# Optimization experiments

Measured on AMD Instinct MI355X. Metric: run time of the kernel, lower is better.

## Reference

```python
import jax, jax.numpy as jnp
import numpy as np
from jax import lax

DN = ('NHWC', 'HWIO', 'NHWC')  # conv dimension numbers


def setup_inputs() -> dict:
    key = jax.random.key(0)
    ks = jax.random.split(key, 10)
    B, H, W, C, F, E = 16, 32, 32, 128, 128, 8
    G = F * (H // 2) * (W // 2)  # 32768, gating flatten size
    return {
        'x': jax.random.normal(ks[0], (B, H, W, C), jnp.float32),
        'eps_kernel': jax.random.normal(ks[1], (3, 3, C, F, E), jnp.float32),
        'eps_gate': jax.random.normal(ks[2], (B, E), jnp.float32),
        'expert_mu': jax.random.normal(ks[3], (3, 3, C, F, E), jnp.float32) * 0.05,
        'expert_rho': jax.random.normal(ks[4], (3, C, F, E), jnp.float32) * 0.01 - 6.0,
        'expert_bias': jax.random.normal(ks[5], (F, E), jnp.float32) * 0.01,
        'gating_kernel': jax.random.normal(ks[6], (3, 3, C, F), jnp.float32) * 0.05,
        'gating_bias': jax.random.normal(ks[7], (F,), jnp.float32) * 0.01,
        'gating_out_kernel': jax.random.normal(ks[8], (G, E), jnp.float32) * 0.01,
        'gating_out_bias': jax.random.normal(ks[9], (E,), jnp.float32) * 0.01,
    }


def reference(x, eps_kernel, eps_gate, expert_mu, expert_rho, expert_bias,
              gating_kernel, gating_bias, gating_out_kernel, gating_out_bias):
    GATING_NOISE_SIGMA = 1e-4
    TOP_K = 2
    B = x.shape[0]
    kh, kw, C, F, E = expert_mu.shape

    # Bayesian reparameterized expert kernels: rho shared over first kernel dim
    sigma = jax.nn.softplus(expert_rho)[None]               # [1,kw,C,F,E]
    kernel = expert_mu + sigma * eps_kernel                 # [kh,kw,C,F,E]

    # All-expert conv as one grouped conv via output-channel packing
    kern_flat = kernel.reshape(kh, kw, C, F * E)
    expert_out = lax.conv_general_dilated(x, kern_flat, (1, 1), 'SAME',
                                          dimension_numbers=DN)
    expert_out = expert_out.reshape(B, x.shape[1], x.shape[2], F, E)
    expert_out = expert_out + expert_bias                   # [B,H,W,F,E]

    # Gating path: conv -> 2x2 maxpool -> flatten -> dense -> noisy logits
    g = lax.conv_general_dilated(x, gating_kernel, (1, 1), 'SAME',
                                 dimension_numbers=DN) + gating_bias
    g = lax.reduce_window(g, -jnp.inf, lax.max,
                          (1, 2, 2, 1), (1, 2, 2, 1), 'VALID')
    logits = g.reshape(B, -1) @ gating_out_kernel + gating_out_bias  # [B,E]
    logits = logits + GATING_NOISE_SIGMA * eps_gate

    # noisy top-k gating: softmax over selected experts, zero elsewhere
    top_vals, top_idx = lax.top_k(logits, TOP_K)
    top_w = jax.nn.softmax(top_vals, axis=-1)
    gates = jnp.zeros((B, E), logits.dtype).at[
        jnp.arange(B)[:, None], top_idx].set(top_w)

    # combine experts weighted by gates, broadcast over spatial dims
    out = jnp.einsum('bhwfe,be->bhwf', expert_out, gates)
    return out
```

## Files before the change

kernel.cpp:

```cpp
#include <hip/hip_runtime.h>
#include <cmath>

#define B_ 16
#define H_ 32
#define W_ 32
#define C_ 128
#define F_ 128
#define KSZ (9*C_*F_)
#define NKS 36
#define FRAG_ELE 4096

typedef __bf16 bf16;
typedef __bf16 bf16x4 __attribute__((ext_vector_type(4)));
typedef __bf16 bf16x8 __attribute__((ext_vector_type(8)));
typedef float  f32x4  __attribute__((ext_vector_type(4)));

__device__ __forceinline__ float softplus_f(float v) {
  return log1pf(expf(-fabsf(v))) + fmaxf(v, 0.f);
}

__device__ __forceinline__ void top2_gates_f(const float* lg, float* gl) {
  int i0 = 0;
  #pragma unroll
  for (int e = 1; e < 8; ++e) if (lg[e] > lg[i0]) i0 = e;
  int i1 = (i0 == 0) ? 1 : 0;
  #pragma unroll
  for (int e = 0; e < 8; ++e) if (e != i0 && lg[e] > lg[i1]) i1 = e;
  float m  = fmaxf(lg[i0], lg[i1]);
  float e0 = expf(lg[i0] - m), e1 = expf(lg[i1] - m);
  float s  = e0 + e1;
  #pragma unroll
  for (int e = 0; e < 8; ++e) gl[e] = 0.f;
  gl[i0] = e0 / s; gl[i1] = e1 / s;
}

__device__ __forceinline__ float logit_f(const float* part, const float* gob,
                                         const float* epsg, int bb, int e) {
  float s = 0.f;
  #pragma unroll
  for (int hb = 0; hb < 16; ++hb) s += part[(bb*16 + hb)*8 + e];
  return s + gob[e] + 1e-4f * epsg[bb*8 + e];
}

__device__ __forceinline__ void block_map_f(int bid, int* b, int* hb) {
  *b  = (bid & 7) * 2 + (bid >> 7);
  *hb = (bid >> 3) & 15;
}

template<int NVAR>
__global__ __launch_bounds__(512, 2) void conv_k(
    const float* __restrict__ x,
    const bf16* __restrict__ Bhi, const bf16* __restrict__ Blo,
    const float* __restrict__ gb,
    const float* __restrict__ Wg,
    const float* __restrict__ part,
    const float* __restrict__ gob,
    const float* __restrict__ epsg,
    const float* __restrict__ ebias,
    float* __restrict__ outv)
{
  int b, hb;
  block_map_f(blockIdx.x, &b, &hb);
  const int t = threadIdx.x;

  __shared__ bf16 xs[NVAR*4*34*128];
  __shared__ float red[8][8];
  __shared__ float gl8[8];

  for (int v = t; v < 4*34*32; v += 512) {
    int c4   = v & 31;
    int col  = (v >> 5) % 34;
    int rowi = (v >> 5) / 34;
    int row  = hb*2 - 1 + rowi;
    int w    = col - 1;
    float4 xv = make_float4(0.f, 0.f, 0.f, 0.f);
    if (row >= 0 && row < H_ && w >= 0 && w < W_)
      xv = *(const float4*)&x[((b*H_ + row)*W_ + w)*C_ + c4*4];
    float vv[4] = {xv.x, xv.y, xv.z, xv.w};
    bf16x4 h4, l4;
    #pragma unroll
    for (int j = 0; j < 4; ++j) {
      h4[j] = (bf16)vv[j];
      if (NVAR == 2) l4[j] = (bf16)(vv[j] - (float)h4[j]);
    }
    int base = ((rowi*34 + col)*256 + c4*8) ^ ((col & 7) << 4);
    *(bf16x4*)((char*)xs + base) = h4;
    if (NVAR == 2) *(bf16x4*)((char*)xs + 34816 + base) = l4;
  }
  if (NVAR == 1 && t == 0) {
    float lg[8], gg[8];
    #pragma unroll
    for (int e = 0; e < 8; ++e) lg[e] = logit_f(part, gob, epsg, b, e);
    top2_gates_f(lg, gg);
    #pragma unroll
    for (int e = 0; e < 8; ++e) gl8[e] = gg[e];
  }
  __syncthreads();

  const int l    = t & 63;
  const int wid  = t >> 6;
  const int mpar = wid & 1;
  const int nf0  = (wid >> 1) << 1;
  const int r15  = l & 15;
  const int q    = l >> 4;

  f32x4 acc00 = {0.f,0.f,0.f,0.f}, acc01 = acc00, acc10 = acc00, acc11 = acc00;

  const bf16* Bh = Bhi + (NVAR == 1 ? (size_t)b * KSZ : (size_t)0);
  const size_t bgo = (size_t)(nf0*512 + l*8);

  bf16x8 s0h0,s0h1,s0l0,s0l1, s1h0,s1h1,s1l0,s1l1, s2h0,s2h1,s2l0,s2l1;

#define LOADB(S, KS_) do {                                                  \
    int kk_ = (KS_); if (kk_ > NKS-1) kk_ = NKS-1;                          \
    size_t o_ = bgo + (size_t)kk_ * FRAG_ELE;                               \
    S##h0 = *(const bf16x8*)(Bh + o_);                                      \
    S##h1 = *(const bf16x8*)(Bh + o_ + 512);                                \
    if (NVAR == 2) {                                                        \
      S##l0 = *(const bf16x8*)(Blo + o_);                                   \
      S##l1 = *(const bf16x8*)(Blo + o_ + 512);                             \
    }                                                                       \
  } while (0)

#define MFMA16(a, bb_, c) __builtin_amdgcn_mfma_f32_16x16x32_bf16(a, bb_, c, 0, 0, 0)

#define COMPUTE(S, KS_) do {                                                \
    const int khkw_ = (KS_) >> 2;                                           \
    const int kh_ = khkw_ / 3, kw_ = khkw_ % 3;                             \
    const int c0_ = ((KS_) & 3) << 5;                                       \
    const int col_ = mpar*16 + r15 + kw_;                                   \
    const int off_ = ((kh_*34 + col_)*256 + (c0_ + q*8)*2) ^ ((col_ & 7) << 4); \
    bf16x8 a0_ = *(const bf16x8*)((const char*)xs + off_);                  \
    bf16x8 a1_ = *(const bf16x8*)((const char*)xs + off_ + 8704);           \
    __builtin_amdgcn_s_setprio(1);                                          \
    acc00 = MFMA16(a0_, S##h0, acc00);                                      \
    acc01 = MFMA16(a0_, S##h1, acc01);                                      \
    acc10 = MFMA16(a1_, S##h0, acc10);                                      \
    acc11 = MFMA16(a1_, S##h1, acc11);                                      \
    if (NVAR == 2) {                                                        \
      bf16x8 g0_ = *(const bf16x8*)((const char*)xs + 34816 + off_);        \
      bf16x8 g1_ = *(const bf16x8*)((const char*)xs + 34816 + off_ + 8704); \
      acc00 = MFMA16(g0_, S##h0, acc00);                                    \
      acc01 = MFMA16(g0_, S##h1, acc01);                                    \
      acc10 = MFMA16(g1_, S##h0, acc10);                                    \
      acc11 = MFMA16(g1_, S##h1, acc11);                                    \
      acc00 = MFMA16(a0_, S##l0, acc00);                                    \
      acc01 = MFMA16(a0_, S##l1, acc01);                                    \
      acc10 = MFMA16(a1_, S##l0, acc10);                                    \
      acc11 = MFMA16(a1_, S##l1, acc11);                                    \
    }                                                                       \
    __builtin_amdgcn_s_setprio(0);                                          \
  } while (0)

  LOADB(s0, 0); LOADB(s1, 1); LOADB(s2, 2);
  for (int ks = 0; ks < NKS; ks += 3) {
    COMPUTE(s0, ks);   LOADB(s0, ks+3);
    COMPUTE(s1, ks+1); LOADB(s1, ks+4);
    COMPUTE(s2, ks+2); LOADB(s2, ks+5);
  }
#undef LOADB
#undef COMPUTE

  if (NVAR == 1) {
    const int f0 = nf0*16 + r15;
    float bv0 = 0.f, bv1 = 0.f;
    #pragma unroll
    for (int e = 0; e < 8; ++e) {
      bv0 += gl8[e] * ebias[f0*8 + e];
      bv1 += gl8[e] * ebias[(f0+16)*8 + e];
    }
    #pragma unroll
    for (int mi = 0; mi < 2; ++mi) {
      const int h = hb*2 + mi;
      #pragma unroll
      for (int r = 0; r < 4; ++r) {
        const int wo = mpar*16 + q*4 + r;
        float* o = &outv[((b*H_ + h)*W_ + wo)*F_];
        o[f0]      = (mi ? acc10[r] : acc00[r]) + bv0;
        o[f0 + 16] = (mi ? acc11[r] : acc01[r]) + bv1;
      }
    }
  } else {
    float pr[8] = {0,0,0,0,0,0,0,0};
    #pragma unroll
    for (int ni = 0; ni < 2; ++ni) {
      const int f = (nf0 + ni)*16 + r15;
      const float bv = gb[f];
      #pragma unroll
      for (int pp = 0; pp < 2; ++pp) {
        float m0 = ni ? fmaxf(acc01[2*pp], acc01[2*pp+1])
                      : fmaxf(acc00[2*pp], acc00[2*pp+1]);
        float m1 = ni ? fmaxf(acc11[2*pp], acc11[2*pp+1])
                      : fmaxf(acc10[2*pp], acc10[2*pp+1]);
        float pm = fmaxf(m0, m1) + bv;
        const int pw = mpar*8 + q*2 + pp;
        const float* wr = &Wg[(size_t)((hb*16 + pw)*128 + f) * 8];
        float4 wA = *(const float4*)wr;
        float4 wB = *(const float4*)(wr + 4);
        pr[0] += pm*wA.x; pr[1] += pm*wA.y; pr[2] += pm*wA.z; pr[3] += pm*wA.w;
        pr[4] += pm*wB.x; pr[5] += pm*wB.y; pr[6] += pm*wB.z; pr[7] += pm*wB.w;
      }
    }
    #pragma unroll
    for (int o = 32; o > 0; o >>= 1)
      #pragma unroll
      for (int e = 0; e < 8; ++e) pr[e] += __shfl_down(pr[e], o);
    if (l == 0)
      #pragma unroll
      for (int e = 0; e < 8; ++e) red[wid][e] = pr[e];
    __syncthreads();
    if (t < 8) {
      float s = 0.f;
      #pragma unroll
      for (int w = 0; w < 8; ++w) s += red[w][t];
      outv[(b*16 + hb)*8 + t] = s;
    }
  }
}

__global__ __launch_bounds__(256) void effk_k(
    const float* __restrict__ mu, const float* __restrict__ rho,
    const float* __restrict__ eps,
    const float* __restrict__ part, const float* __restrict__ gob,
    const float* __restrict__ epsg,
    bf16* __restrict__ Bg)
{
  const int ks  = blockIdx.x >> 3;
  const int rem = blockIdx.x & 7;
  const int t   = threadIdx.x;
  const int nf  = (rem & 1)*4 + (t >> 6);
  const int bq  = (rem >> 1) * 4;

  __shared__ float lgs[4][8];
  __shared__ float gl[4][8];
  if (t < 32) lgs[t >> 3][t & 7] = logit_f(part, gob, epsg, bq + (t >> 3), t & 7);
  __syncthreads();
  if (t < 4) top2_gates_f(lgs[t], gl[t]);
  __syncthreads();

  const int l    = t & 63;
  const int khkw = ks >> 2;
  const int kw   = khkw % 3;
  const int f    = nf*16 + (l & 15);
  const int cb   = (ks & 3)*32 + (l >> 4)*8;

  bf16x8 ob[4];
  #pragma unroll
  for (int j = 0; j < 8; ++j) {
    const int c = cb + j;
    const float* mp = &mu [(size_t)((khkw*C_ + c)*F_ + f) * 8];
    const float* ep = &eps[(size_t)((khkw*C_ + c)*F_ + f) * 8];
    const float* rp = &rho[(size_t)((kw  *C_ + c)*F_ + f) * 8];
    float kv[8];
    #pragma unroll
    for (int e = 0; e < 8; ++e)
      kv[e] = mp[e] + softplus_f(rp[e]) * ep[e];
    #pragma unroll
    for (int bb = 0; bb < 4; ++bb) {
      float s = 0.f;
      #pragma unroll
      for (int e = 0; e < 8; ++e) s += gl[bb][e] * kv[e];
      ob[bb][j] = (bf16)s;
    }
  }
  #pragma unroll
  for (int bb = 0; bb < 4; ++bb) {
    size_t o = (size_t)(bq + bb)*KSZ + (size_t)ks*FRAG_ELE + nf*512 + l*8;
    *(bf16x8*)&Bg[o] = ob[bb];
  }
}

__global__ __launch_bounds__(512) void gkconv_k(
    const float* __restrict__ gk, bf16* __restrict__ bgh, bf16* __restrict__ bgl)
{
  __shared__ float tile[32*129];
  const int ks   = blockIdx.x;
  const int khkw = ks >> 2;
  const int cb   = (ks & 3)*32;
  const int t    = threadIdx.x;

  for (int v = t; v < 1024; v += 512) {
    int c  = v >> 5;
    int f4 = (v & 31) * 4;
    float4 val = *(const float4*)&gk[(size_t)(khkw*C_ + cb + c)*F_ + f4];
    float* dst = &tile[c*129 + f4];
    dst[0] = val.x; dst[1] = val.y; dst[2] = val.z; dst[3] = val.w;
  }
  __syncthreads();

  const int nf = t >> 6, l = t & 63;
  const int f  = nf*16 + (l & 15);
  bf16x8 h8, l8;
  #pragma unroll
  for (int j = 0; j < 8; ++j) {
    int c = (l >> 4)*8 + j;
    float v = tile[c*129 + f];
    bf16 h = (bf16)v;
    h8[j] = h;
    l8[j] = (bf16)(v - (float)h);
  }
  *(bf16x8*)&bgh[(size_t)ks*FRAG_ELE + t*8] = h8;
  *(bf16x8*)&bgl[(size_t)ks*FRAG_ELE + t*8] = l8;
}

extern "C" void kernel_launch(void* const* d_in, const int* in_sizes, int n_in,
                              void* d_out, int out_size, void* d_ws, size_t ws_size,
                              hipStream_t stream) {
  const float* x    = (const float*)d_in[0];
  const float* epsk = (const float*)d_in[1];
  const float* epsg = (const float*)d_in[2];
  const float* mu   = (const float*)d_in[3];
  const float* rho  = (const float*)d_in[4];
  const float* ebias= (const float*)d_in[5];
  const float* gk   = (const float*)d_in[6];
  const float* gb   = (const float*)d_in[7];
  const float* gok  = (const float*)d_in[8];
  const float* gob  = (const float*)d_in[9];
  float* out = (float*)d_out;

  char* ws = (char*)d_ws;
  bf16*  bgh  = (bf16*) (ws);
  bf16*  bgl  = (bf16*) (ws + 294912);
  bf16*  bge  = (bf16*) (ws + 589824);
  float* part = (float*)(ws + 5308416);

  gkconv_k<<<NKS, 512, 0, stream>>>(gk, bgh, bgl);
  conv_k<2><<<B_*16, 512, 0, stream>>>(x, bgh, bgl, gb, gok,
                                       nullptr, nullptr, nullptr, nullptr, part);
  effk_k<<<NKS*8, 256, 0, stream>>>(mu, rho, epsk, part, gob, epsg, bge);
  conv_k<1><<<B_*16, 512, 0, stream>>>(x, bge, bge, nullptr, nullptr,
                                       part, gob, epsg, ebias, out);
}
```

Measured before the change: 65.72 us.

## Split conv blocks over output-channel halves and redistribute waves across rows

Doubles the conv grid so each block computes only half of the output channels, and gives each wave one output row with 32 channels instead of two rows. This halves the per-wave accumulators and raises the launch-bounds occupancy hint, so all CUs get more concurrent waves. The gating max-pool now combines the two rows through shared memory, and the partial-logit buffer grows to 32 slices per batch. The cost is that each block stages the input tile into LDS twice as often overall, and the pooling path adds extra barriers.

```diff
diff --git a/kernel.cpp b/kernel.cpp
--- a/kernel.cpp
+++ b/kernel.cpp
@@ -38,17 +38,18 @@
                                          const float* epsg, int bb, int e) {
   float s = 0.f;
   #pragma unroll
-  for (int hb = 0; hb < 16; ++hb) s += part[(bb*16 + hb)*8 + e];
+  for (int p = 0; p < 32; ++p) s += part[(bb*32 + p)*8 + e];
   return s + gob[e] + 1e-4f * epsg[bb*8 + e];
 }
 
-__device__ __forceinline__ void block_map_f(int bid, int* b, int* hb) {
-  *b  = (bid & 7) * 2 + (bid >> 7);
+__device__ __forceinline__ void block_map_f(int bid, int* b, int* hb, int* nh) {
+  *b  = (bid & 7) * 2 + (bid >> 8);
   *hb = (bid >> 3) & 15;
+  *nh = (bid >> 7) & 1;
 }
 
 template<int NVAR>
-__global__ __launch_bounds__(512, 2) void conv_k(
+__global__ __launch_bounds__(512, 4) void conv_k(
     const float* __restrict__ x,
     const bf16* __restrict__ Bhi, const bf16* __restrict__ Blo,
     const float* __restrict__ gb,
@@ -59,8 +60,8 @@
     const float* __restrict__ ebias,
     float* __restrict__ outv)
 {
-  int b, hb;
-  block_map_f(blockIdx.x, &b, &hb);
+  int b, hb, nh;
+  block_map_f(blockIdx.x, &b, &hb, &nh);
   const int t = threadIdx.x;
 
   __shared__ bf16 xs[NVAR*4*34*128];
@@ -99,15 +100,17 @@
 
   const int l    = t & 63;
   const int wid  = t >> 6;
-  const int mpar = wid & 1;
-  const int nf0  = (wid >> 1) << 1;
+  const int mq   = wid & 3;
+  const int hl   = mq >> 1;
+  const int wh   = mq & 1;
+  const int nfp  = wid >> 2;
   const int r15  = l & 15;
   const int q    = l >> 4;
 
-  f32x4 acc00 = {0.f,0.f,0.f,0.f}, acc01 = acc00, acc10 = acc00, acc11 = acc00;
+  f32x4 acc0 = {0.f,0.f,0.f,0.f}, acc1 = acc0;
 
   const bf16* Bh = Bhi + (NVAR == 1 ? (size_t)b * KSZ : (size_t)0);
-  const size_t bgo = (size_t)(nf0*512 + l*8);
+  const size_t bgo = (size_t)((nh*4 + nfp*2)*512 + l*8);
 
   bf16x8 s0h0,s0h1,s0l0,s0l1, s1h0,s1h1,s1l0,s1l1, s2h0,s2h1,s2l0,s2l1;
 
@@ -128,26 +131,19 @@
     const int khkw_ = (KS_) >> 2;                                           \
     const int kh_ = khkw_ / 3, kw_ = khkw_ % 3;                             \
     const int c0_ = ((KS_) & 3) << 5;                                       \
-    const int col_ = mpar*16 + r15 + kw_;                                   \
-    const int off_ = ((kh_*34 + col_)*256 + (c0_ + q*8)*2) ^ ((col_ & 7) << 4); \
-    bf16x8 a0_ = *(const bf16x8*)((const char*)xs + off_);                  \
-    bf16x8 a1_ = *(const bf16x8*)((const char*)xs + off_ + 8704);           \
+    const int col_ = wh*16 + r15 + kw_;                                     \
+    const int off_ = (((kh_ + hl)*34 + col_)*256 + (c0_ + q*8)*2)           \
+                     ^ ((col_ & 7) << 4);                                   \
+    bf16x8 a_hi = *(const bf16x8*)((const char*)xs + off_);                 \
     __builtin_amdgcn_s_setprio(1);                                          \
-    acc00 = MFMA16(a0_, S##h0, acc00);                                      \
-    acc01 = MFMA16(a0_, S##h1, acc01);                                      \
-    acc10 = MFMA16(a1_, S##h0, acc10);                                      \
-    acc11 = MFMA16(a1_, S##h1, acc11);                                      \
+    acc0 = MFMA16(a_hi, S##h0, acc0);                                       \
+    acc1 = MFMA16(a_hi, S##h1, acc1);                                       \
     if (NVAR == 2) {                                                        \
-      bf16x8 g0_ = *(const bf16x8*)((const char*)xs + 34816 + off_);        \
-      bf16x8 g1_ = *(const bf16x8*)((const char*)xs + 34816 + off_ + 8704); \
-      acc00 = MFMA16(g0_, S##h0, acc00);                                    \
-      acc01 = MFMA16(g0_, S##h1, acc01);                                    \
-      acc10 = MFMA16(g1_, S##h0, acc10);                                    \
-      acc11 = MFMA16(g1_, S##h1, acc11);                                    \
-      acc00 = MFMA16(a0_, S##l0, acc00);                                    \
-      acc01 = MFMA16(a0_, S##l1, acc01);                                    \
-      acc10 = MFMA16(a1_, S##l0, acc10);                                    \
-      acc11 = MFMA16(a1_, S##l1, acc11);                                    \
+      bf16x8 a_lo = *(const bf16x8*)((const char*)xs + 34816 + off_);       \
+      acc0 = MFMA16(a_lo, S##h0, acc0);                                     \
+      acc1 = MFMA16(a_lo, S##h1, acc1);                                     \
+      acc0 = MFMA16(a_hi, S##l0, acc0);                                     \
+      acc1 = MFMA16(a_hi, S##l1, acc1);                                     \
     }                                                                       \
     __builtin_amdgcn_s_setprio(0);                                          \
   } while (0)
@@ -162,43 +158,52 @@
 #undef COMPUTE
 
   if (NVAR == 1) {
-    const int f0 = nf0*16 + r15;
+    const int f0 = nh*64 + nfp*32 + r15;
     float bv0 = 0.f, bv1 = 0.f;
     #pragma unroll
     for (int e = 0; e < 8; ++e) {
       bv0 += gl8[e] * ebias[f0*8 + e];
       bv1 += gl8[e] * ebias[(f0+16)*8 + e];
     }
-    #pragma unroll
-    for (int mi = 0; mi < 2; ++mi) {
-      const int h = hb*2 + mi;
-      #pragma unroll
-      for (int r = 0; r < 4; ++r) {
-        const int wo = mpar*16 + q*4 + r;
-        float* o = &outv[((b*H_ + h)*W_ + wo)*F_];
-        o[f0]      = (mi ? acc10[r] : acc00[r]) + bv0;
-        o[f0 + 16] = (mi ? acc11[r] : acc01[r]) + bv1;
+    const int h = hb*2 + hl;
+    #pragma unroll
+    for (int r = 0; r < 4; ++r) {
+      const int wo = wh*16 + q*4 + r;
+      float* o = &outv[((b*H_ + h)*W_ + wo)*F_];
+      o[f0]      = acc0[r] + bv0;
+      o[f0 + 16] = acc1[r] + bv1;
+    }
+  } else {
+    __syncthreads();
+    float* hpool = (float*)xs;
+    #pragma unroll
+    for (int ni = 0; ni < 2; ++ni) {
+      const int fl = nfp*32 + ni*16 + r15;
+      #pragma unroll
+      for (int pp = 0; pp < 2; ++pp) {
+        float mw = ni ? fmaxf(acc1[2*pp], acc1[2*pp+1])
+                      : fmaxf(acc0[2*pp], acc0[2*pp+1]);
+        const int pw = wh*8 + q*2 + pp;
+        hpool[(hl*16 + pw)*64 + fl] = mw;
       }
     }
-  } else {
+    __syncthreads();
     float pr[8] = {0,0,0,0,0,0,0,0};
-    #pragma unroll
-    for (int ni = 0; ni < 2; ++ni) {
-      const int f = (nf0 + ni)*16 + r15;
-      const float bv = gb[f];
-      #pragma unroll
-      for (int pp = 0; pp < 2; ++pp) {
-        float m0 = ni ? fmaxf(acc01[2*pp], acc01[2*pp+1])
-                      : fmaxf(acc00[2*pp], acc00[2*pp+1]);
-        float m1 = ni ? fmaxf(acc11[2*pp], acc11[2*pp+1])
-                      : fmaxf(acc10[2*pp], acc10[2*pp+1]);
-        float pm = fmaxf(m0, m1) + bv;
-        const int pw = mpar*8 + q*2 + pp;
-        const float* wr = &Wg[(size_t)((hb*16 + pw)*128 + f) * 8];
-        float4 wA = *(const float4*)wr;
-        float4 wB = *(const float4*)(wr + 4);
-        pr[0] += pm*wA.x; pr[1] += pm*wA.y; pr[2] += pm*wA.z; pr[3] += pm*wA.w;
-        pr[4] += pm*wB.x; pr[5] += pm*wB.y; pr[6] += pm*wB.z; pr[7] += pm*wB.w;
+    if (hl == 0) {
+      #pragma unroll
+      for (int ni = 0; ni < 2; ++ni) {
+        const int fl = nfp*32 + ni*16 + r15;
+        const float bv = gb[nh*64 + fl];
+        #pragma unroll
+        for (int pp = 0; pp < 2; ++pp) {
+          const int pw = wh*8 + q*2 + pp;
+          float pm = fmaxf(hpool[pw*64 + fl], hpool[(16 + pw)*64 + fl]) + bv;
+          const float* wr = &Wg[(size_t)((hb*16 + pw)*128 + nh*64 + fl) * 8];
+          float4 wA = *(const float4*)wr;
+          float4 wB = *(const float4*)(wr + 4);
+          pr[0] += pm*wA.x; pr[1] += pm*wA.y; pr[2] += pm*wA.z; pr[3] += pm*wA.w;
+          pr[4] += pm*wB.x; pr[5] += pm*wB.y; pr[6] += pm*wB.z; pr[7] += pm*wB.w;
+        }
       }
     }
     #pragma unroll
@@ -213,7 +218,7 @@
       float s = 0.f;
       #pragma unroll
       for (int w = 0; w < 8; ++w) s += red[w][t];
-      outv[(b*16 + hb)*8 + t] = s;
+      outv[(b*32 + hb*2 + nh)*8 + t] = s;
     }
   }
 }
@@ -325,9 +330,9 @@
   float* part = (float*)(ws + 5308416);
 
   gkconv_k<<<NKS, 512, 0, stream>>>(gk, bgh, bgl);
-  conv_k<2><<<B_*16, 512, 0, stream>>>(x, bgh, bgl, gb, gok,
-                                       nullptr, nullptr, nullptr, nullptr, part);
+  conv_k<2><<<512, 512, 0, stream>>>(x, bgh, bgl, gb, gok,
+                                     nullptr, nullptr, nullptr, nullptr, part);
   effk_k<<<NKS*8, 256, 0, stream>>>(mu, rho, epsk, part, gob, epsg, bge);
-  conv_k<1><<<B_*16, 512, 0, stream>>>(x, bge, bge, nullptr, nullptr,
-                                       part, gob, epsg, ebias, out);
-}
+  conv_k<1><<<512, 512, 0, stream>>>(x, bge, bge, nullptr, nullptr,
+                                     part, gob, epsg, ebias, out);
+}
```

Measured after the change: 78.62 us. 19.6% more time.

## Stage conv weight fragments through LDS with async global_load_lds pipeline

Applied to the files above, without the earlier changes.

The conv kernel now has each wave issue global_load_lds copies of one weight fragment per K-step into a ring buffer in shared memory. The pipeline is 6 deep for the expert conv and 3 deep for the gating conv, with vmcnt waits plus a block barrier each step. Previously each wave loaded its own fragments into registers, so every fragment was fetched twice, by both waves sharing an nf pair; now each is fetched once and shared. The occupancy hint of 2 blocks per CU is dropped, and the new per-step barrier adds sync cost. Separately, effk_k handles 8 batches per block instead of 4, halving the grid and reusing the computed expert kernel values across more batches.

```diff
diff --git a/kernel.cpp b/kernel.cpp
--- a/kernel.cpp
+++ b/kernel.cpp
@@ -48,7 +48,7 @@
 }
 
 template<int NVAR>
-__global__ __launch_bounds__(512, 2) void conv_k(
+__global__ __launch_bounds__(512) void conv_k(
     const float* __restrict__ x,
     const bf16* __restrict__ Bhi, const bf16* __restrict__ Blo,
     const float* __restrict__ gb,
@@ -59,13 +59,40 @@
     const float* __restrict__ ebias,
     float* __restrict__ outv)
 {
+  constexpr int DEP   = (NVAR == 1) ? 6 : 3;
+  constexpr int RDEP  = DEP + 1;
+  constexpr int SLOTE = (NVAR == 1) ? 4096 : 8192;
+
   int b, hb;
   block_map_f(blockIdx.x, &b, &hb);
-  const int t = threadIdx.x;
+  const int t   = threadIdx.x;
+  const int l   = t & 63;
+  const int wid = t >> 6;
 
   __shared__ bf16 xs[NVAR*4*34*128];
+  __shared__ bf16 bB[RDEP * SLOTE];
   __shared__ float red[8][8];
   __shared__ float gl8[8];
+
+  const bf16* Bh = Bhi + (NVAR == 1 ? (size_t)b * KSZ : (size_t)0);
+
+#define STAGE(KS_) do {                                                     \
+    int kk_ = (KS_) < NKS ? (KS_) : NKS-1;                                  \
+    int sl_ = ((KS_) % RDEP) * SLOTE + wid*512;                             \
+    const bf16* gs_ = Bh + (size_t)kk_*FRAG_ELE + wid*512 + l*8;            \
+    __builtin_amdgcn_global_load_lds(                                       \
+        (const __attribute__((address_space(1))) void*)gs_,                 \
+        (__attribute__((address_space(3))) void*)&bB[sl_], 16, 0, 0);       \
+    if (NVAR == 2) {                                                        \
+      const bf16* g2_ = Blo + (size_t)kk_*FRAG_ELE + wid*512 + l*8;         \
+      __builtin_amdgcn_global_load_lds(                                     \
+          (const __attribute__((address_space(1))) void*)g2_,               \
+          (__attribute__((address_space(3))) void*)&bB[sl_ + 4096], 16, 0, 0); \
+    }                                                                       \
+  } while (0)
+
+  #pragma unroll
+  for (int d = 0; d < DEP; ++d) STAGE(d);
 
   for (int v = t; v < 4*34*32; v += 512) {
     int c4   = v & 31;
@@ -97,8 +124,6 @@
   }
   __syncthreads();
 
-  const int l    = t & 63;
-  const int wid  = t >> 6;
   const int mpar = wid & 1;
   const int nf0  = (wid >> 1) << 1;
   const int r15  = l & 15;
@@ -106,60 +131,51 @@
 
   f32x4 acc00 = {0.f,0.f,0.f,0.f}, acc01 = acc00, acc10 = acc00, acc11 = acc00;
 
-  const bf16* Bh = Bhi + (NVAR == 1 ? (size_t)b * KSZ : (size_t)0);
-  const size_t bgo = (size_t)(nf0*512 + l*8);
-
-  bf16x8 s0h0,s0h1,s0l0,s0l1, s1h0,s1h1,s1l0,s1l1, s2h0,s2h1,s2l0,s2l1;
-
-#define LOADB(S, KS_) do {                                                  \
-    int kk_ = (KS_); if (kk_ > NKS-1) kk_ = NKS-1;                          \
-    size_t o_ = bgo + (size_t)kk_ * FRAG_ELE;                               \
-    S##h0 = *(const bf16x8*)(Bh + o_);                                      \
-    S##h1 = *(const bf16x8*)(Bh + o_ + 512);                                \
-    if (NVAR == 2) {                                                        \
-      S##l0 = *(const bf16x8*)(Blo + o_);                                   \
-      S##l1 = *(const bf16x8*)(Blo + o_ + 512);                             \
-    }                                                                       \
-  } while (0)
-
 #define MFMA16(a, bb_, c) __builtin_amdgcn_mfma_f32_16x16x32_bf16(a, bb_, c, 0, 0, 0)
 
-#define COMPUTE(S, KS_) do {                                                \
-    const int khkw_ = (KS_) >> 2;                                           \
-    const int kh_ = khkw_ / 3, kw_ = khkw_ % 3;                             \
-    const int c0_ = ((KS_) & 3) << 5;                                       \
-    const int col_ = mpar*16 + r15 + kw_;                                   \
-    const int off_ = ((kh_*34 + col_)*256 + (c0_ + q*8)*2) ^ ((col_ & 7) << 4); \
-    bf16x8 a0_ = *(const bf16x8*)((const char*)xs + off_);                  \
-    bf16x8 a1_ = *(const bf16x8*)((const char*)xs + off_ + 8704);           \
-    __builtin_amdgcn_s_setprio(1);                                          \
-    acc00 = MFMA16(a0_, S##h0, acc00);                                      \
-    acc01 = MFMA16(a0_, S##h1, acc01);                                      \
-    acc10 = MFMA16(a1_, S##h0, acc10);                                      \
-    acc11 = MFMA16(a1_, S##h1, acc11);                                      \
-    if (NVAR == 2) {                                                        \
-      bf16x8 g0_ = *(const bf16x8*)((const char*)xs + 34816 + off_);        \
-      bf16x8 g1_ = *(const bf16x8*)((const char*)xs + 34816 + off_ + 8704); \
-      acc00 = MFMA16(g0_, S##h0, acc00);                                    \
-      acc01 = MFMA16(g0_, S##h1, acc01);                                    \
-      acc10 = MFMA16(g1_, S##h0, acc10);                                    \
-      acc11 = MFMA16(g1_, S##h1, acc11);                                    \
-      acc00 = MFMA16(a0_, S##l0, acc00);                                    \
-      acc01 = MFMA16(a0_, S##l1, acc01);                                    \
-      acc10 = MFMA16(a1_, S##l0, acc10);                                    \
-      acc11 = MFMA16(a1_, S##l1, acc11);                                    \
-    }                                                                       \
-    __builtin_amdgcn_s_setprio(0);                                          \
-  } while (0)
-
-  LOADB(s0, 0); LOADB(s1, 1); LOADB(s2, 2);
-  for (int ks = 0; ks < NKS; ks += 3) {
-    COMPUTE(s0, ks);   LOADB(s0, ks+3);
-    COMPUTE(s1, ks+1); LOADB(s1, ks+4);
-    COMPUTE(s2, ks+2); LOADB(s2, ks+5);
-  }
-#undef LOADB
-#undef COMPUTE
+  for (int ks = 0; ks < NKS; ++ks) {
+    if (NVAR == 1) asm volatile("s_waitcnt vmcnt(5)" ::: "memory");
+    else           asm volatile("s_waitcnt vmcnt(4)" ::: "memory");
+    __builtin_amdgcn_s_barrier();
+
+    const int sb = (ks % RDEP) * SLOTE;
+    bf16x8 bh0 = *(const bf16x8*)&bB[sb + nf0*512 + l*8];
+    bf16x8 bh1 = *(const bf16x8*)&bB[sb + (nf0+1)*512 + l*8];
+
+    const int khkw = ks >> 2;
+    const int kh = khkw / 3, kw = khkw % 3;
+    const int c0 = (ks & 3) << 5;
+    const int col = mpar*16 + r15 + kw;
+    const int off = ((kh*34 + col)*256 + (c0 + q*8)*2) ^ ((col & 7) << 4);
+    bf16x8 a0 = *(const bf16x8*)((const char*)xs + off);
+    bf16x8 a1 = *(const bf16x8*)((const char*)xs + off + 8704);
+
+    STAGE(ks + DEP);
+
+    __builtin_amdgcn_s_setprio(1);
+    acc00 = MFMA16(a0, bh0, acc00);
+    acc01 = MFMA16(a0, bh1, acc01);
+    acc10 = MFMA16(a1, bh0, acc10);
+    acc11 = MFMA16(a1, bh1, acc11);
+    if (NVAR == 2) {
+      bf16x8 bl0 = *(const bf16x8*)&bB[sb + 4096 + nf0*512 + l*8];
+      bf16x8 bl1 = *(const bf16x8*)&bB[sb + 4096 + (nf0+1)*512 + l*8];
+      bf16x8 g0  = *(const bf16x8*)((const char*)xs + 34816 + off);
+      bf16x8 g1  = *(const bf16x8*)((const char*)xs + 34816 + off + 8704);
+      acc00 = MFMA16(g0, bh0, acc00);
+      acc01 = MFMA16(g0, bh1, acc01);
+      acc10 = MFMA16(g1, bh0, acc10);
+      acc11 = MFMA16(g1, bh1, acc11);
+      acc00 = MFMA16(a0, bl0, acc00);
+      acc01 = MFMA16(a0, bl1, acc01);
+      acc10 = MFMA16(a1, bl0, acc10);
+      acc11 = MFMA16(a1, bl1, acc11);
+    }
+    __builtin_amdgcn_s_setprio(0);
+  }
+#undef STAGE
+#undef MFMA16
+  asm volatile("s_waitcnt vmcnt(0)" ::: "memory");
 
   if (NVAR == 1) {
     const int f0 = nf0*16 + r15;
@@ -225,17 +241,17 @@
     const float* __restrict__ epsg,
     bf16* __restrict__ Bg)
 {
-  const int ks  = blockIdx.x >> 3;
-  const int rem = blockIdx.x & 7;
+  const int ks  = blockIdx.x >> 2;
+  const int rem = blockIdx.x & 3;
   const int t   = threadIdx.x;
   const int nf  = (rem & 1)*4 + (t >> 6);
-  const int bq  = (rem >> 1) * 4;
-
-  __shared__ float lgs[4][8];
-  __shared__ float gl[4][8];
-  if (t < 32) lgs[t >> 3][t & 7] = logit_f(part, gob, epsg, bq + (t >> 3), t & 7);
+  const int bq  = (rem >> 1) * 8;
+
+  __shared__ float lgs[8][8];
+  __shared__ float gl[8][8];
+  if (t < 64) lgs[t >> 3][t & 7] = logit_f(part, gob, epsg, bq + (t >> 3), t & 7);
   __syncthreads();
-  if (t < 4) top2_gates_f(lgs[t], gl[t]);
+  if (t < 8) top2_gates_f(lgs[t], gl[t]);
   __syncthreads();
 
   const int l    = t & 63;
@@ -244,7 +260,7 @@
   const int f    = nf*16 + (l & 15);
   const int cb   = (ks & 3)*32 + (l >> 4)*8;
 
-  bf16x8 ob[4];
+  bf16x8 ob[8];
   #pragma unroll
   for (int j = 0; j < 8; ++j) {
     const int c = cb + j;
@@ -256,7 +272,7 @@
     for (int e = 0; e < 8; ++e)
       kv[e] = mp[e] + softplus_f(rp[e]) * ep[e];
     #pragma unroll
-    for (int bb = 0; bb < 4; ++bb) {
+    for (int bb = 0; bb < 8; ++bb) {
       float s = 0.f;
       #pragma unroll
       for (int e = 0; e < 8; ++e) s += gl[bb][e] * kv[e];
@@ -264,7 +280,7 @@
     }
   }
   #pragma unroll
-  for (int bb = 0; bb < 4; ++bb) {
+  for (int bb = 0; bb < 8; ++bb) {
     size_t o = (size_t)(bq + bb)*KSZ + (size_t)ks*FRAG_ELE + nf*512 + l*8;
     *(bf16x8*)&Bg[o] = ob[bb];
   }
@@ -327,7 +343,7 @@
   gkconv_k<<<NKS, 512, 0, stream>>>(gk, bgh, bgl);
   conv_k<2><<<B_*16, 512, 0, stream>>>(x, bgh, bgl, gb, gok,
                                        nullptr, nullptr, nullptr, nullptr, part);
-  effk_k<<<NKS*8, 256, 0, stream>>>(mu, rho, epsk, part, gob, epsg, bge);
+  effk_k<<<NKS*4, 256, 0, stream>>>(mu, rho, epsk, part, gob, epsg, bge);
   conv_k<1><<<B_*16, 512, 0, stream>>>(x, bge, bge, nullptr, nullptr,
                                        part, gob, epsg, ebias, out);
 }
```

After: 70.26 us. 1.07x slower.

## Split conv reduction dimension across two warp groups with LDS combine

Applied to the files above, without the earlier changes.

Doubles the conv block to 1024 threads and splits the 36 k-steps between two groups of 8 waves. Each group accumulates half the reduction, then the second group writes its partial accumulators to shared memory and the first group adds them before the epilogue. The aim is more waves in flight to hide the latency of B-fragment loads, since the grid is only 256 blocks. The cost is extra LDS traffic, two additional barriers, and tighter register limits from the 1024/4 launch bounds.

```diff
diff --git a/kernel.cpp b/kernel.cpp
--- a/kernel.cpp
+++ b/kernel.cpp
@@ -48,7 +48,7 @@
 }
 
 template<int NVAR>
-__global__ __launch_bounds__(512, 2) void conv_k(
+__global__ __launch_bounds__(1024, 4) void conv_k(
     const float* __restrict__ x,
     const bf16* __restrict__ Bhi, const bf16* __restrict__ Blo,
     const float* __restrict__ gb,
@@ -61,13 +61,17 @@
 {
   int b, hb;
   block_map_f(blockIdx.x, &b, &hb);
-  const int t = threadIdx.x;
+  const int t   = threadIdx.x;
+  const int l   = t & 63;
+  const int wid = t >> 6;
+  const int kg  = wid >> 3;
+  const int w8  = wid & 7;
 
   __shared__ bf16 xs[NVAR*4*34*128];
   __shared__ float red[8][8];
   __shared__ float gl8[8];
 
-  for (int v = t; v < 4*34*32; v += 512) {
+  for (int v = t; v < 4*34*32; v += 1024) {
     int c4   = v & 31;
     int col  = (v >> 5) % 34;
     int rowi = (v >> 5) / 34;
@@ -97,10 +101,8 @@
   }
   __syncthreads();
 
-  const int l    = t & 63;
-  const int wid  = t >> 6;
-  const int mpar = wid & 1;
-  const int nf0  = (wid >> 1) << 1;
+  const int mpar = w8 & 1;
+  const int nf0  = (w8 >> 1) << 1;
   const int r15  = l & 15;
   const int q    = l >> 4;
 
@@ -152,8 +154,9 @@
     __builtin_amdgcn_s_setprio(0);                                          \
   } while (0)
 
-  LOADB(s0, 0); LOADB(s1, 1); LOADB(s2, 2);
-  for (int ks = 0; ks < NKS; ks += 3) {
+  const int ks0 = kg * (NKS/2);
+  LOADB(s0, ks0); LOADB(s1, ks0+1); LOADB(s2, ks0+2);
+  for (int ks = ks0; ks < ks0 + NKS/2; ks += 3) {
     COMPUTE(s0, ks);   LOADB(s0, ks+3);
     COMPUTE(s1, ks+1); LOADB(s1, ks+4);
     COMPUTE(s2, ks+2); LOADB(s2, ks+5);
@@ -161,53 +164,79 @@
 #undef LOADB
 #undef COMPUTE
 
+  __syncthreads();
+  float* comb = (float*)xs;
+  if (kg == 1) {
+    #pragma unroll
+    for (int r = 0; r < 4; ++r) {
+      comb[(w8*16 + 0  + r)*64 + l] = acc00[r];
+      comb[(w8*16 + 4  + r)*64 + l] = acc01[r];
+      comb[(w8*16 + 8  + r)*64 + l] = acc10[r];
+      comb[(w8*16 + 12 + r)*64 + l] = acc11[r];
+    }
+  }
+  __syncthreads();
+  if (kg == 0) {
+    #pragma unroll
+    for (int r = 0; r < 4; ++r) {
+      acc00[r] += comb[(w8*16 + 0  + r)*64 + l];
+      acc01[r] += comb[(w8*16 + 4  + r)*64 + l];
+      acc10[r] += comb[(w8*16 + 8  + r)*64 + l];
+      acc11[r] += comb[(w8*16 + 12 + r)*64 + l];
+    }
+  }
+
   if (NVAR == 1) {
-    const int f0 = nf0*16 + r15;
-    float bv0 = 0.f, bv1 = 0.f;
-    #pragma unroll
-    for (int e = 0; e < 8; ++e) {
-      bv0 += gl8[e] * ebias[f0*8 + e];
-      bv1 += gl8[e] * ebias[(f0+16)*8 + e];
-    }
-    #pragma unroll
-    for (int mi = 0; mi < 2; ++mi) {
-      const int h = hb*2 + mi;
-      #pragma unroll
-      for (int r = 0; r < 4; ++r) {
-        const int wo = mpar*16 + q*4 + r;
-        float* o = &outv[((b*H_ + h)*W_ + wo)*F_];
-        o[f0]      = (mi ? acc10[r] : acc00[r]) + bv0;
-        o[f0 + 16] = (mi ? acc11[r] : acc01[r]) + bv1;
+    if (kg == 0) {
+      const int f0 = nf0*16 + r15;
+      float bv0 = 0.f, bv1 = 0.f;
+      #pragma unroll
+      for (int e = 0; e < 8; ++e) {
+        bv0 += gl8[e] * ebias[f0*8 + e];
+        bv1 += gl8[e] * ebias[(f0+16)*8 + e];
+      }
+      #pragma unroll
+      for (int mi = 0; mi < 2; ++mi) {
+        const int h = hb*2 + mi;
+        #pragma unroll
+        for (int r = 0; r < 4; ++r) {
+          const int wo = mpar*16 + q*4 + r;
+          float* o = &outv[((b*H_ + h)*W_ + wo)*F_];
+          o[f0]      = (mi ? acc10[r] : acc00[r]) + bv0;
+          o[f0 + 16] = (mi ? acc11[r] : acc01[r]) + bv1;
+        }
       }
     }
   } else {
     float pr[8] = {0,0,0,0,0,0,0,0};
-    #pragma unroll
-    for (int ni = 0; ni < 2; ++ni) {
-      const int f = (nf0 + ni)*16 + r15;
-      const float bv = gb[f];
-      #pragma unroll
-      for (int pp = 0; pp < 2; ++pp) {
-        float m0 = ni ? fmaxf(acc01[2*pp], acc01[2*pp+1])
-                      : fmaxf(acc00[2*pp], acc00[2*pp+1]);
-        float m1 = ni ? fmaxf(acc11[2*pp], acc11[2*pp+1])
-                      : fmaxf(acc10[2*pp], acc10[2*pp+1]);
-        float pm = fmaxf(m0, m1) + bv;
-        const int pw = mpar*8 + q*2 + pp;
-        const float* wr = &Wg[(size_t)((hb*16 + pw)*128 + f) * 8];
-        float4 wA = *(const float4*)wr;
-        float4 wB = *(const float4*)(wr + 4);
-        pr[0] += pm*wA.x; pr[1] += pm*wA.y; pr[2] += pm*wA.z; pr[3] += pm*wA.w;
-        pr[4] += pm*wB.x; pr[5] += pm*wB.y; pr[6] += pm*wB.z; pr[7] += pm*wB.w;
+    if (kg == 0) {
+      #pragma unroll
+      for (int ni = 0; ni < 2; ++ni) {
+        const int f = (nf0 + ni)*16 + r15;
+        const float bv = gb[f];
+        #pragma unroll
+        for (int pp = 0; pp < 2; ++pp) {
+          float m0 = ni ? fmaxf(acc01[2*pp], acc01[2*pp+1])
+                        : fmaxf(acc00[2*pp], acc00[2*pp+1]);
+          float m1 = ni ? fmaxf(acc11[2*pp], acc11[2*pp+1])
+                        : fmaxf(acc10[2*pp], acc10[2*pp+1]);
+          float pm = fmaxf(m0, m1) + bv;
+          const int pw = mpar*8 + q*2 + pp;
+          const float* wr = &Wg[(size_t)((hb*16 + pw)*128 + f) * 8];
+          float4 wA = *(const float4*)wr;
+          float4 wB = *(const float4*)(wr + 4);
+          pr[0] += pm*wA.x; pr[1] += pm*wA.y; pr[2] += pm*wA.z; pr[3] += pm*wA.w;
+          pr[4] += pm*wB.x; pr[5] += pm*wB.y; pr[6] += pm*wB.z; pr[7] += pm*wB.w;
+        }
       }
     }
     #pragma unroll
     for (int o = 32; o > 0; o >>= 1)
       #pragma unroll
       for (int e = 0; e < 8; ++e) pr[e] += __shfl_down(pr[e], o);
-    if (l == 0)
-      #pragma unroll
-      for (int e = 0; e < 8; ++e) red[wid][e] = pr[e];
+    if (l == 0 && kg == 0)
+      #pragma unroll
+      for (int e = 0; e < 8; ++e) red[w8][e] = pr[e];
     __syncthreads();
     if (t < 8) {
       float s = 0.f;
@@ -325,9 +354,9 @@
   float* part = (float*)(ws + 5308416);
 
   gkconv_k<<<NKS, 512, 0, stream>>>(gk, bgh, bgl);
-  conv_k<2><<<B_*16, 512, 0, stream>>>(x, bgh, bgl, gb, gok,
-                                       nullptr, nullptr, nullptr, nullptr, part);
+  conv_k<2><<<B_*16, 1024, 0, stream>>>(x, bgh, bgl, gb, gok,
+                                        nullptr, nullptr, nullptr, nullptr, part);
   effk_k<<<NKS*8, 256, 0, stream>>>(mu, rho, epsk, part, gob, epsg, bge);
-  conv_k<1><<<B_*16, 512, 0, stream>>>(x, bge, bge, nullptr, nullptr,
-                                       part, gob, epsg, ebias, out);
-}
+  conv_k<1><<<B_*16, 1024, 0, stream>>>(x, bge, bge, nullptr, nullptr,
+                                        part, gob, epsg, ebias, out);
+}
```

Result: no change. 65.49 us (-0.3%).
